# Performance work log

Hardware: AMD Instinct MI355X
Metric: run time of the kernel (lower is better)

Reference implementation:

```python
import jax, jax.numpy as jnp
import numpy as np

H = 8          # attention heads (all three convs)
N_NODES = 50000
N_EDGES = 800000
IN_DIM = 16
N_GRAPHS = 256


def _gat_layer(x, src, dst, W, a_src, a_dst, b, n_nodes):
    """PyG GATConv (concat=True, add_self_loops handled by caller via src/dst)."""
    f_out = a_src.shape[1]
    h = (x @ W).reshape(n_nodes, H, f_out)              # [N,H,F]
    al_s = jnp.einsum('nhf,hf->nh', h, a_src)           # [N,H]
    al_d = jnp.einsum('nhf,hf->nh', h, a_dst)           # [N,H]
    e = jax.nn.leaky_relu(al_s[src] + al_d[dst], 0.2)   # [E,H] per-edge logits
    # segment softmax over incoming edges of each destination node
    m = jax.ops.segment_max(e, dst, num_segments=n_nodes)
    m = jnp.where(jnp.isfinite(m), m, 0.0)
    p = jnp.exp(e - m[dst])
    s = jax.ops.segment_sum(p, dst, num_segments=n_nodes)
    alpha = p / (s[dst] + 1e-16)                        # [E,H]
    out = jax.ops.segment_sum(h[src] * alpha[:, :, None], dst, num_segments=n_nodes)
    return out.reshape(n_nodes, H * f_out) + b


def setup_inputs() -> dict:
    key = jax.random.key(0)
    ks = jax.random.split(key, 16)
    x = jax.random.normal(ks[0], (N_NODES, IN_DIM), dtype=jnp.float32)
    edge_index = jax.random.randint(ks[1], (2, N_EDGES), 0, N_NODES, dtype=jnp.int64)
    batch = jnp.sort(jax.random.randint(ks[2], (N_NODES,), 0, N_GRAPHS, dtype=jnp.int64))

    def glorot(k, shape):
        fan = shape[0] + shape[-1]
        return jax.random.normal(k, shape, dtype=jnp.float32) * np.sqrt(2.0 / fan)

    # conv1: 16 -> 8 heads x 8
    W1 = glorot(ks[3], (IN_DIM, H * 8))
    a_src1 = glorot(ks[4], (H, 8)); a_dst1 = glorot(ks[5], (H, 8))
    b1 = jnp.zeros((H * 8,), jnp.float32)
    # conv2: 64 -> 8 heads x 16
    W2 = glorot(ks[6], (64, H * 16))
    a_src2 = glorot(ks[7], (H, 16)); a_dst2 = glorot(ks[8], (H, 16))
    b2 = jnp.zeros((H * 16,), jnp.float32)
    # conv3: 128 -> 8 heads x 16
    W3 = glorot(ks[9], (128, H * 16))
    a_src3 = glorot(ks[10], (H, 16)); a_dst3 = glorot(ks[11], (H, 16))
    b3 = jnp.zeros((H * 16,), jnp.float32)

    fc1_w = glorot(ks[12], (128, 32)); fc1_b = jnp.zeros((32,), jnp.float32)
    fc2_w = glorot(ks[13], (32, 1));   fc2_b = jnp.zeros((1,), jnp.float32)

    return dict(x=x, edge_index=edge_index, batch=batch,
                W1=W1, a_src1=a_src1, a_dst1=a_dst1, b1=b1,
                W2=W2, a_src2=a_src2, a_dst2=a_dst2, b2=b2,
                W3=W3, a_src3=a_src3, a_dst3=a_dst3, b3=b3,
                fc1_w=fc1_w, fc1_b=fc1_b, fc2_w=fc2_w, fc2_b=fc2_b)


def reference(x, edge_index, batch,
              W1, a_src1, a_dst1, b1,
              W2, a_src2, a_dst2, b2,
              W3, a_src3, a_dst3, b3,
              fc1_w, fc1_b, fc2_w, fc2_b):
    n = x.shape[0]
    loops = jnp.arange(n, dtype=edge_index.dtype)        # GATConv add_self_loops=True
    src = jnp.concatenate([edge_index[0], loops])
    dst = jnp.concatenate([edge_index[1], loops])

    # eval mode: the F.dropout calls are no-ops
    h = jax.nn.elu(_gat_layer(x, src, dst, W1, a_src1, a_dst1, b1, n))
    h = jax.nn.elu(_gat_layer(h, src, dst, W2, a_src2, a_dst2, b2, n))
    h = jax.nn.elu(_gat_layer(h, src, dst, W3, a_src3, a_dst3, b3, n))

    # global_mean_pool over graph ids
    cnt = jax.ops.segment_sum(jnp.ones((n,), h.dtype), batch, num_segments=N_GRAPHS)
    pooled = jax.ops.segment_sum(h, batch, num_segments=N_GRAPHS) / jnp.maximum(cnt, 1.0)[:, None]

    out = jax.nn.relu(pooled @ fc1_w + fc1_b)
    return out @ fc2_w + fc2_b                            # [N_GRAPHS, 1]
```

## Files before the change

### kernel.cpp

```cpp
#include <hip/hip_runtime.h>
#include <hip/hip_bf16.h>
#include <cstdint>
#include <cstddef>

#define GAT_H 8
#define KBMAX 256
#define BCAP  6144
#define SB    8

typedef short bf16x8 __attribute__((ext_vector_type(8)));
typedef float f32x4  __attribute__((ext_vector_type(4)));

__device__ __forceinline__ unsigned bf16r(float x) {
    const unsigned u = __float_as_uint(x);
    return (u + 0x7fffu + ((u >> 16) & 1u)) >> 16;
}
#define B2F_LO(u) __uint_as_float((u) << 16)
#define B2F_HI(u) __uint_as_float((u) & 0xffff0000u)


__global__ __launch_bounds__(256) void bkt_scatter(const int* __restrict__ ei,
                                                   int* __restrict__ bwoff,
                                                   unsigned* __restrict__ staging,
                                                   float* __restrict__ Mh,
                                                   int nE, int nN, int kb) {
    __shared__ int cnt[KBMAX];
    __shared__ int gb[KBMAX];
    const int tid = threadIdx.x;
    if (blockIdx.x == 0 && tid < 3 * GAT_H) Mh[tid] = 0.f;
    cnt[tid] = 0;
    __syncthreads();
    const int base = blockIdx.x * 2048;
    const int ET = nE + nN;
    unsigned pk[8]; int bb[8], lr[8];
    #pragma unroll
    for (int k = 0; k < 8; ++k) {
        const int e = base + k * 256 + tid;
        bb[k] = -1;
        if (e < ET) {
            int src, dst;
            if (e < nE) { src = ei[e]; dst = ei[nE + e]; }
            else        { src = dst = e - nE; }
            pk[k] = ((unsigned)dst << 16) | (unsigned)src;
            bb[k] = dst >> 8;
            lr[k] = atomicAdd(&cnt[bb[k]], 1);
        }
    }
    __syncthreads();
    if (tid < kb)
        gb[tid] = cnt[tid] ? atomicAdd(&bwoff[tid], cnt[tid]) : 0;
    __syncthreads();
    #pragma unroll
    for (int k = 0; k < 8; ++k)
        if (bb[k] >= 0) {
            const int pos = gb[bb[k]] + lr[k];
            if (pos < BCAP)
                staging[(size_t)bb[k] * BCAP + pos] = pk[k];
        }
}

__global__ __launch_bounds__(1024) void bkt_build(const unsigned* __restrict__ staging,
                                                  const int* __restrict__ bwoff,
                                                  int* __restrict__ rowptr,
                                                  int* __restrict__ esrc, int N, int kb) {
    __shared__ int hist[256 * SB];
    __shared__ int run[256 * SB];
    __shared__ int sc[KBMAX];
    __shared__ int wt[4];
    __shared__ int wsum[16];
    __shared__ int outv[BCAP];
    const int b = blockIdx.x;
    const int tid = threadIdx.x;
    const int lane = tid & 63, wid = tid >> 6;

    if (tid < KBMAX) sc[tid] = (tid < kb) ? bwoff[tid] : 0;
    for (int i = tid; i < 256 * SB; i += 1024) { hist[i] = 0; run[i] = 0; }
    __syncthreads();

    if (tid < 256) {
        int incl = sc[tid];
        #pragma unroll
        for (int d = 1; d < 64; d <<= 1) {
            const int t2 = __shfl_up(incl, d, 64);
            if (lane >= d) incl += t2;
        }
        if (lane == 63) wt[wid] = incl;
        sc[tid] = incl;
    }
    __syncthreads();
    if (tid < 256) {
        int add = 0;
        #pragma unroll
        for (int w = 0; w < 4; ++w) if (w < wid) add += wt[w];
        sc[tid] += add;
    }
    __syncthreads();
    const int lo   = b ? sc[b - 1] : 0;
    const int cntb = sc[b] - lo;
    const int d0 = b << 8;
    const int nd = min(256, N - d0);
    const unsigned* stg = staging + (size_t)b * BCAP;
    const int lim = min(cntb, BCAP);

    for (int i = tid; i < lim; i += 1024) {
        const unsigned p = stg[i];
        const int dl = (int)(p >> 16) - d0;
        const int q  = (int)(p & 0xffffu) >> 13;
        atomicAdd(&hist[dl * SB + q], 1);
    }
    __syncthreads();

    const int b0 = hist[2 * tid], b1 = hist[2 * tid + 1];
    const int ps = b0 + b1;
    int incl = ps;
    #pragma unroll
    for (int d = 1; d < 64; d <<= 1) {
        const int t2 = __shfl_up(incl, d, 64);
        if (lane >= d) incl += t2;
    }
    if (lane == 63) wsum[wid] = incl;
    __syncthreads();
    if (tid == 0) {
        int runng = 0;
        #pragma unroll
        for (int w = 0; w < 16; ++w) { const int t2 = wsum[w]; wsum[w] = runng; runng += t2; }
    }
    __syncthreads();
    const int excl = wsum[wid] + incl - ps;
    hist[2 * tid]     = excl;
    hist[2 * tid + 1] = excl + b0;
    __syncthreads();

    if (tid < nd)
        rowptr[d0 + tid + 1] = lo + ((tid < 255) ? hist[(tid + 1) * SB] : cntb);
    if (b == 0 && tid == 0) rowptr[0] = 0;

    for (int i = tid; i < lim; i += 1024) {
        const unsigned p = stg[i];
        const int dl = (int)(p >> 16) - d0;
        const int q  = (int)(p & 0xffffu) >> 13;
        const int bin = dl * SB + q;
        const int pos = hist[bin] + atomicAdd(&run[bin], 1);
        if (pos < BCAP) outv[pos] = (int)(p & 0xffffu);
    }
    __syncthreads();
    for (int i = tid; i < lim; i += 1024) esrc[lo + i] = outv[i];
}


__global__ void wconv_kernel(const float* __restrict__ W, unsigned short* __restrict__ Wt, int D) {
    const int t = blockIdx.x * blockDim.x + threadIdx.x;
    if (t >= 128 * D) return;
    const int c = t / D, k = t % D;
    Wt[t] = (unsigned short)bf16r(W[(size_t)k * 128 + c]);
}


template<int D>
__global__ __launch_bounds__(256) void matmul_mfma(
        const unsigned short* __restrict__ X,
        const unsigned short* __restrict__ Wt,
        unsigned short* __restrict__ Hb,
        int N) {
    constexpr int DP = D + 8;
    __shared__ unsigned short xs[64 * DP];
    __shared__ unsigned short wsh[128 * DP];
    const int tid = threadIdx.x;
    const int n0 = blockIdx.x * 64;

    for (int t = tid; t < 64 * (D / 8); t += 256) {
        const int row = t / (D / 8), c8 = (t % (D / 8)) * 8;
        const int n = n0 + row;
        uint4 u = make_uint4(0u, 0u, 0u, 0u);
        if (n < N) u = *reinterpret_cast<const uint4*>(&X[(size_t)n * D + c8]);
        *reinterpret_cast<uint4*>(&xs[row * DP + c8]) = u;
    }
    for (int t = tid; t < 128 * (D / 8); t += 256) {
        const int row = t / (D / 8), c8 = (t % (D / 8)) * 8;
        *reinterpret_cast<uint4*>(&wsh[row * DP + c8]) =
            *reinterpret_cast<const uint4*>(&Wt[(size_t)row * D + c8]);
    }
    __syncthreads();

    const int w = tid >> 6, l = tid & 63;
    const int lr = l & 15, lk = l >> 4;
    f32x4 acc[8];
    #pragma unroll
    for (int j = 0; j < 8; ++j) acc[j] = (f32x4){0.f, 0.f, 0.f, 0.f};

    #pragma unroll
    for (int ks = 0; ks < D / 32; ++ks) {
        const int kb = ks * 32 + lk * 8;
        const bf16x8 a = *reinterpret_cast<const bf16x8*>(&xs[(16 * w + lr) * DP + kb]);
        #pragma unroll
        for (int nt = 0; nt < 8; ++nt) {
            const bf16x8 bfr = *reinterpret_cast<const bf16x8*>(&wsh[(16 * nt + lr) * DP + kb]);
            acc[nt] = __builtin_amdgcn_mfma_f32_16x16x32_bf16(a, bfr, acc[nt], 0, 0, 0);
        }
    }

    #pragma unroll
    for (int nt = 0; nt < 8; ++nt) {
        #pragma unroll
        for (int r = 0; r < 4; ++r) {
            const int n = n0 + 16 * w + lk * 4 + r;
            if (n < N)
                Hb[(size_t)n * 128 + 16 * nt + lr] = (unsigned short)bf16r(acc[nt][r]);
        }
    }
}


__global__ __launch_bounds__(256) void attnlogit_kernel(
        const unsigned short* __restrict__ Hb,
        const float* __restrict__ a_src, const float* __restrict__ a_dst,
        float* __restrict__ als, float* __restrict__ ald,
        float* __restrict__ Mh, int N) {
    __shared__ float sh[256];
    const int t = blockIdx.x * 256 + threadIdx.x;
    const int tid = threadIdx.x;
    float s1 = -1e30f;
    if (t < N * GAT_H) {
        const int h = t & 7;
        union { uint4 q[2]; unsigned w[8]; } v;
        const uint4* hp = reinterpret_cast<const uint4*>(Hb + (size_t)t * 16);
        v.q[0] = hp[0]; v.q[1] = hp[1];
        float a1 = 0.f, a2 = 0.f;
        #pragma unroll
        for (int j = 0; j < 8; ++j) {
            const float lo = B2F_LO(v.w[j]), hi2 = B2F_HI(v.w[j]);
            a1 += lo * a_src[h * 16 + 2 * j] + hi2 * a_src[h * 16 + 2 * j + 1];
            a2 += lo * a_dst[h * 16 + 2 * j] + hi2 * a_dst[h * 16 + 2 * j + 1];
        }
        als[t] = a1; ald[t] = a2;
        s1 = a1;
    }
    sh[tid] = s1;
    __syncthreads();
    #pragma unroll
    for (int off = 128; off >= 8; off >>= 1) {
        if (tid < off) sh[tid] = fmaxf(sh[tid], sh[tid + off]);
        __syncthreads();
    }
    if (tid < 8) {
        const float v2 = sh[tid];
        if (v2 > 0.f) atomicMax((int*)&Mh[tid], __float_as_int(v2));
    }
}


template<int D, int C, int KK, int F>
__global__ __launch_bounds__(256) void matmul_fused(
        const float* __restrict__ X, const float* __restrict__ W,
        const float* __restrict__ a_src, const float* __restrict__ a_dst,
        unsigned short* __restrict__ Hb,
        float* __restrict__ als, float* __restrict__ ald,
        float* __restrict__ Mh, int N) {
    constexpr int CG  = C / 8;
    constexpr int NGR = 256 / CG;
    constexpr int NPT = 64 / NGR;
    constexpr int XS  = KK + 4;
    __shared__ float xs[64][XS];
    __shared__ float wsh[KK][C];
    __shared__ int bmax[GAT_H];

    const int n0 = blockIdx.x * 64;
    const int tid = threadIdx.x;
    const int cg = tid % CG, ngr = tid / CG;
    const int c0 = cg * 8;
    if (tid < GAT_H) bmax[tid] = 0;

    float acc[NPT][8];
    #pragma unroll
    for (int i = 0; i < NPT; ++i)
        #pragma unroll
        for (int j = 0; j < 8; ++j) acc[i][j] = 0.f;

    for (int k0 = 0; k0 < D; k0 += KK) {
        for (int t = tid; t < 64 * (KK / 4); t += 256) {
            const int row = t / (KK / 4), c4 = (t % (KK / 4)) * 4;
            const int n = n0 + row;
            float4 v = make_float4(0.f, 0.f, 0.f, 0.f);
            if (n < N) v = *reinterpret_cast<const float4*>(&X[(size_t)n * D + k0 + c4]);
            *reinterpret_cast<float4*>(&xs[row][c4]) = v;
        }
        for (int t = tid; t < KK * (C / 4); t += 256) {
            const int row = t / (C / 4), c4 = (t % (C / 4)) * 4;
            *reinterpret_cast<float4*>(&wsh[row][c4]) =
                *reinterpret_cast<const float4*>(&W[(size_t)(k0 + row) * C + c4]);
        }
        __syncthreads();

        #pragma unroll
        for (int k4 = 0; k4 < KK; k4 += 4) {
            float4 xv[NPT];
            #pragma unroll
            for (int i = 0; i < NPT; ++i)
                xv[i] = *reinterpret_cast<const float4*>(&xs[ngr * NPT + i][k4]);
            #pragma unroll
            for (int kk = 0; kk < 4; ++kk) {
                const float4 w0 = *reinterpret_cast<const float4*>(&wsh[k4 + kk][c0]);
                const float4 w1 = *reinterpret_cast<const float4*>(&wsh[k4 + kk][c0 + 4]);
                #pragma unroll
                for (int i = 0; i < NPT; ++i) {
                    const float xk = (kk == 0) ? xv[i].x : (kk == 1) ? xv[i].y
                                   : (kk == 2) ? xv[i].z : xv[i].w;
                    acc[i][0] += xk * w0.x; acc[i][1] += xk * w0.y;
                    acc[i][2] += xk * w0.z; acc[i][3] += xk * w0.w;
                    acc[i][4] += xk * w1.x; acc[i][5] += xk * w1.y;
                    acc[i][6] += xk * w1.z; acc[i][7] += xk * w1.w;
                }
            }
        }
        __syncthreads();
    }

    const int h   = c0 / F;
    float asr[8], adr[8];
    #pragma unroll
    for (int q = 0; q < 8; ++q) {
        asr[q] = a_src[h * F + q];
        adr[q] = a_dst[h * F + q];
    }

    #pragma unroll
    for (int i = 0; i < NPT; ++i) {
        float s = 0.f, d2 = 0.f;
        #pragma unroll
        for (int q = 0; q < 8; ++q) { s += acc[i][q] * asr[q]; d2 += acc[i][q] * adr[q]; }
        const int n = n0 + ngr * NPT + i;
        if (n < N) {
            uint4 pk;
            pk.x = bf16r(acc[i][0]) | (bf16r(acc[i][1]) << 16);
            pk.y = bf16r(acc[i][2]) | (bf16r(acc[i][3]) << 16);
            pk.z = bf16r(acc[i][4]) | (bf16r(acc[i][5]) << 16);
            pk.w = bf16r(acc[i][6]) | (bf16r(acc[i][7]) << 16);
            *reinterpret_cast<uint4*>(&Hb[(size_t)n * C + c0]) = pk;
            als[(size_t)n * GAT_H + h] = s;
            ald[(size_t)n * GAT_H + h] = d2;
            if (s > 0.f) atomicMax(&bmax[h], __float_as_int(s));
        }
    }
    __syncthreads();
    if (tid < GAT_H) {
        const int v = bmax[tid];
        if (v > 0) atomicMax((int*)&Mh[tid], v);
    }
}


template<int F>
__global__ void gat_gather(const int* __restrict__ rowptr, const int* __restrict__ esrc,
                           const float* __restrict__ als, const float* __restrict__ ald,
                           const float* __restrict__ Mh,
                           const unsigned short* __restrict__ Hb, const float* __restrict__ b,
                           unsigned short* __restrict__ outb, int N) {
    const int t = blockIdx.x * blockDim.x + threadIdx.x;
    if (t >= N * GAT_H) return;
    const int dst = t >> 3, h = t & 7;
    const int beg = rowptr[dst], end = rowptr[dst + 1];
    const float adh = ald[t];
    float bnd = Mh[h] + adh;
    bnd = bnd > 0.f ? bnd : 0.2f * bnd;

    constexpr int NW = F / 2;
    float s = 0.f;
    float acc[F];
    #pragma unroll
    for (int j = 0; j < F; ++j) acc[j] = 0.f;

    int i = beg;
    for (; i + 1 < end; i += 2) {
        const int sa = esrc[i], sb = esrc[i + 1];
        const float ala = als[sa * GAT_H + h];
        const float alb = als[sb * GAT_H + h];
        union { uint4 q[NW / 4]; unsigned w[NW]; } va, vb;
        const uint4* ha  = reinterpret_cast<const uint4*>(Hb + ((size_t)sa * GAT_H + h) * F);
        const uint4* hb2 = reinterpret_cast<const uint4*>(Hb + ((size_t)sb * GAT_H + h) * F);
        #pragma unroll
        for (int j = 0; j < NW / 4; ++j) { va.q[j] = ha[j]; vb.q[j] = hb2[j]; }

        float xa = ala + adh; xa = xa > 0.f ? xa : 0.2f * xa;
        float xb = alb + adh; xb = xb > 0.f ? xb : 0.2f * xb;
        const float pa = __expf(xa - bnd);
        const float pb = __expf(xb - bnd);
        s += pa + pb;
        #pragma unroll
        for (int j = 0; j < NW; ++j) {
            acc[2 * j]     += pa * B2F_LO(va.w[j]) + pb * B2F_LO(vb.w[j]);
            acc[2 * j + 1] += pa * B2F_HI(va.w[j]) + pb * B2F_HI(vb.w[j]);
        }
    }
    if (i < end) {
        const int sa = esrc[i];
        const float ala = als[sa * GAT_H + h];
        union { uint4 q[NW / 4]; unsigned w[NW]; } va;
        const uint4* ha = reinterpret_cast<const uint4*>(Hb + ((size_t)sa * GAT_H + h) * F);
        #pragma unroll
        for (int j = 0; j < NW / 4; ++j) va.q[j] = ha[j];
        float xa = ala + adh; xa = xa > 0.f ? xa : 0.2f * xa;
        const float pa = __expf(xa - bnd);
        s += pa;
        #pragma unroll
        for (int j = 0; j < NW; ++j) {
            acc[2 * j]     += pa * B2F_LO(va.w[j]);
            acc[2 * j + 1] += pa * B2F_HI(va.w[j]);
        }
    }

    const float inv = 1.f / s;
    float val[F];
    #pragma unroll
    for (int j = 0; j < F; ++j) {
        const float v = acc[j] * inv + b[h * F + j];
        val[j] = v > 0.f ? v : expm1f(v);
    }
    #pragma unroll
    for (int j8 = 0; j8 < F / 8; ++j8) {
        uint4 pk;
        pk.x = bf16r(val[8 * j8 + 0]) | (bf16r(val[8 * j8 + 1]) << 16);
        pk.y = bf16r(val[8 * j8 + 2]) | (bf16r(val[8 * j8 + 3]) << 16);
        pk.z = bf16r(val[8 * j8 + 4]) | (bf16r(val[8 * j8 + 5]) << 16);
        pk.w = bf16r(val[8 * j8 + 6]) | (bf16r(val[8 * j8 + 7]) << 16);
        *reinterpret_cast<uint4*>(&outb[((size_t)dst * GAT_H + h) * F + 8 * j8]) = pk;
    }
}


__global__ __launch_bounds__(256) void pool_mlp_kernel(
        const unsigned short* __restrict__ Ab, const int* __restrict__ batch,
        const float* __restrict__ fc1w, const float* __restrict__ fc1b,
        const float* __restrict__ fc2w, const float* __restrict__ fc2b,
        float* __restrict__ out, int N) {
    const int g = blockIdx.x;
    int lo, hi;
    {
        int l = 0, h2 = N;
        while (l < h2) { const int mid = (l + h2) >> 1; if (batch[mid] < g) l = mid + 1; else h2 = mid; }
        lo = l;
        h2 = N;
        while (l < h2) { const int mid = (l + h2) >> 1; if (batch[mid] < g + 1) l = mid + 1; else h2 = mid; }
        hi = l;
    }
    __shared__ float part[16][128];
    __shared__ float pl[128];
    __shared__ float red2[32];
    const int tid = threadIdx.x;
    const int c8 = (tid & 15) * 8, r = tid >> 4;
    float a8[8];
    #pragma unroll
    for (int j = 0; j < 8; ++j) a8[j] = 0.f;
    for (int n = lo + r; n < hi; n += 16) {
        const uint4 u = *reinterpret_cast<const uint4*>(&Ab[(size_t)n * 128 + c8]);
        a8[0] += B2F_LO(u.x); a8[1] += B2F_HI(u.x);
        a8[2] += B2F_LO(u.y); a8[3] += B2F_HI(u.y);
        a8[4] += B2F_LO(u.z); a8[5] += B2F_HI(u.z);
        a8[6] += B2F_LO(u.w); a8[7] += B2F_HI(u.w);
    }
    #pragma unroll
    for (int j = 0; j < 8; ++j) part[r][c8 + j] = a8[j];
    __syncthreads();
    if (tid < 128) {
        float s = 0.f;
        #pragma unroll
        for (int rr = 0; rr < 16; ++rr) s += part[rr][tid];
        pl[tid] = s / fmaxf((float)(hi - lo), 1.f);
    }
    __syncthreads();
    if (tid < 32) {
        float a = fc1b[tid];
        for (int k = 0; k < 128; ++k) a += pl[k] * fc1w[k * 32 + tid];
        a = fmaxf(a, 0.f);
        red2[tid] = a * fc2w[tid];
    }
    __syncthreads();
    if (tid == 0) {
        float sum = fc2b[0];
        for (int k = 0; k < 32; ++k) sum += red2[k];
        out[g] = sum;
    }
}


extern "C" void kernel_launch(void* const* d_in, const int* in_sizes, int n_in,
                              void* d_out, int out_size, void* d_ws, size_t ws_size,
                              hipStream_t stream) {
    const float* x     = (const float*)d_in[0];
    const int*   ei    = (const int*)  d_in[1];
    const int*   batch = (const int*)  d_in[2];
    const float* W1 = (const float*)d_in[3],  *as1 = (const float*)d_in[4],
               *ad1 = (const float*)d_in[5],  *b1  = (const float*)d_in[6];
    const float* W2 = (const float*)d_in[7],  *as2 = (const float*)d_in[8],
               *ad2 = (const float*)d_in[9],  *b2  = (const float*)d_in[10];
    const float* W3 = (const float*)d_in[11], *as3 = (const float*)d_in[12],
               *ad3 = (const float*)d_in[13], *b3  = (const float*)d_in[14];
    const float* fc1w = (const float*)d_in[15], *fc1b = (const float*)d_in[16];
    const float* fc2w = (const float*)d_in[17], *fc2b = (const float*)d_in[18];

    const int N  = in_sizes[0] / 16;
    const int NE = in_sizes[1] / 2;
    const int NG = out_size;
    const int ET = NE + N;
    const int KB = (N + 255) >> 8;

    float* ws = (float*)d_ws;
    size_t off = 0;
    unsigned short* Ab = (unsigned short*)(ws + off); off += (size_t)N * 64;
    unsigned short* Hb = (unsigned short*)(ws + off); off += (size_t)N * 64;
    float* als  = ws + off; off += (size_t)N * GAT_H;
    float* ald  = ws + off; off += (size_t)N * GAT_H;
    float* Mh   = ws + off; off += 3 * GAT_H;
    int* rowptr = (int*)(ws + off); off += N + 1;
    int* esrc   = (int*)(ws + off); off += ET;
    unsigned* staging = (unsigned*)(ws + off); off += (size_t)KB * BCAP;
    int* bwoff  = (int*)(ws + off); off += KBMAX;
    unsigned short* Wt2 = (unsigned short*)(ws + off); off += 128 * 64 / 2;
    unsigned short* Wt3 = (unsigned short*)(ws + off); off += 128 * 128 / 2;

    hipMemsetAsync(bwoff, 0, KBMAX * sizeof(int), stream);
    bkt_scatter<<<(ET + 2047) / 2048, 256, 0, stream>>>(ei, bwoff, staging, Mh, NE, N, KB);
    bkt_build<<<KB, 1024, 0, stream>>>(staging, bwoff, rowptr, esrc, N, KB);
    wconv_kernel<<<(128 * 64 + 255) / 256, 256, 0, stream>>>(W2, Wt2, 64);
    wconv_kernel<<<(128 * 128 + 255) / 256, 256, 0, stream>>>(W3, Wt3, 128);

    const int NH = N * GAT_H;
    const int NHB = (NH + 255) / 256;
    const int NB = (N + 63) / 64;

    matmul_fused<16, 64, 16, 8><<<NB, 256, 0, stream>>>(x, W1, as1, ad1, Hb, als, ald, Mh, N);
    gat_gather<8><<<NHB, 256, 0, stream>>>(rowptr, esrc, als, ald, Mh, Hb, b1, Ab, N);

    matmul_mfma<64><<<NB, 256, 0, stream>>>(Ab, Wt2, Hb, N);
    attnlogit_kernel<<<NHB, 256, 0, stream>>>(Hb, as2, ad2, als, ald, Mh + GAT_H, N);
    gat_gather<16><<<NHB, 256, 0, stream>>>(rowptr, esrc, als, ald, Mh + GAT_H, Hb, b2, Ab, N);

    matmul_mfma<128><<<NB, 256, 0, stream>>>(Ab, Wt3, Hb, N);
    attnlogit_kernel<<<NHB, 256, 0, stream>>>(Hb, as3, ad3, als, ald, Mh + 2 * GAT_H, N);
    gat_gather<16><<<NHB, 256, 0, stream>>>(rowptr, esrc, als, ald, Mh + 2 * GAT_H, Hb, b3, Ab, N);

    pool_mlp_kernel<<<NG, 256, 0, stream>>>(Ab, batch, fc1w, fc1b, fc2w, fc2b,
                                            (float*)d_out, N);
}
```

Measured before the change: 233.1 us.

## Fuse attention-logit computation into MFMA matmul and coalesce H stores via LDS

Measured after the change: 218.5 us (median of 2 runs). 1.07x faster.

```diff
diff --git a/kernel.cpp b/kernel.cpp
--- a/kernel.cpp
+++ b/kernel.cpp
@@ -160,13 +160,19 @@
 __global__ __launch_bounds__(256) void matmul_mfma(
         const unsigned short* __restrict__ X,
         const unsigned short* __restrict__ Wt,
+        const float* __restrict__ a_src, const float* __restrict__ a_dst,
         unsigned short* __restrict__ Hb,
-        int N) {
+        float* __restrict__ als, float* __restrict__ ald,
+        float* __restrict__ Mh, int N) {
     constexpr int DP = D + 8;
+    constexpr int OP = 136;
+    static_assert(128 * DP >= 64 * OP, "wsh reuse too small");
     __shared__ unsigned short xs[64 * DP];
     __shared__ unsigned short wsh[128 * DP];
+    __shared__ int bmax[GAT_H];
     const int tid = threadIdx.x;
     const int n0 = blockIdx.x * 64;
+    if (tid < GAT_H) bmax[tid] = 0;
 
     for (int t = tid; t < 64 * (D / 8); t += 256) {
         const int row = t / (D / 8), c8 = (t % (D / 8)) * 8;
@@ -198,53 +204,56 @@
             acc[nt] = __builtin_amdgcn_mfma_f32_16x16x32_bf16(a, bfr, acc[nt], 0, 0, 0);
         }
     }
-
+    __syncthreads();
+
+    float asr[8], adr[8];
     #pragma unroll
     for (int nt = 0; nt < 8; ++nt) {
-        #pragma unroll
-        for (int r = 0; r < 4; ++r) {
-            const int n = n0 + 16 * w + lk * 4 + r;
-            if (n < N)
-                Hb[(size_t)n * 128 + 16 * nt + lr] = (unsigned short)bf16r(acc[nt][r]);
-        }
-    }
-}
-
-
-__global__ __launch_bounds__(256) void attnlogit_kernel(
-        const unsigned short* __restrict__ Hb,
-        const float* __restrict__ a_src, const float* __restrict__ a_dst,
-        float* __restrict__ als, float* __restrict__ ald,
-        float* __restrict__ Mh, int N) {
-    __shared__ float sh[256];
-    const int t = blockIdx.x * 256 + threadIdx.x;
-    const int tid = threadIdx.x;
-    float s1 = -1e30f;
-    if (t < N * GAT_H) {
-        const int h = t & 7;
-        union { uint4 q[2]; unsigned w[8]; } v;
-        const uint4* hp = reinterpret_cast<const uint4*>(Hb + (size_t)t * 16);
-        v.q[0] = hp[0]; v.q[1] = hp[1];
-        float a1 = 0.f, a2 = 0.f;
-        #pragma unroll
-        for (int j = 0; j < 8; ++j) {
-            const float lo = B2F_LO(v.w[j]), hi2 = B2F_HI(v.w[j]);
-            a1 += lo * a_src[h * 16 + 2 * j] + hi2 * a_src[h * 16 + 2 * j + 1];
-            a2 += lo * a_dst[h * 16 + 2 * j] + hi2 * a_dst[h * 16 + 2 * j + 1];
-        }
-        als[t] = a1; ald[t] = a2;
-        s1 = a1;
-    }
-    sh[tid] = s1;
-    __syncthreads();
-    #pragma unroll
-    for (int off = 128; off >= 8; off >>= 1) {
-        if (tid < off) sh[tid] = fmaxf(sh[tid], sh[tid + off]);
-        __syncthreads();
-    }
-    if (tid < 8) {
-        const float v2 = sh[tid];
-        if (v2 > 0.f) atomicMax((int*)&Mh[tid], __float_as_int(v2));
+        asr[nt] = a_src[nt * 16 + lr];
+        adr[nt] = a_dst[nt * 16 + lr];
+    }
+    float mys[4] = {0.f, 0.f, 0.f, 0.f}, myd[4] = {0.f, 0.f, 0.f, 0.f};
+    #pragma unroll
+    for (int r = 0; r < 4; ++r) {
+        #pragma unroll
+        for (int nt = 0; nt < 8; ++nt) {
+            float ps = acc[nt][r] * asr[nt];
+            float pd = acc[nt][r] * adr[nt];
+            #pragma unroll
+            for (int d = 1; d < 16; d <<= 1) {
+                ps += __shfl_xor(ps, d, 16);
+                pd += __shfl_xor(pd, d, 16);
+            }
+            if (lr == nt) { mys[r] = ps; myd[r] = pd; }
+        }
+    }
+    #pragma unroll
+    for (int r = 0; r < 4; ++r) {
+        const int n = n0 + 16 * w + lk * 4 + r;
+        if (lr < GAT_H && n < N) {
+            als[(size_t)n * GAT_H + lr] = mys[r];
+            ald[(size_t)n * GAT_H + lr] = myd[r];
+            if (mys[r] > 0.f) atomicMax(&bmax[lr], __float_as_int(mys[r]));
+        }
+    }
+
+    unsigned short* trp = wsh;
+    #pragma unroll
+    for (int nt = 0; nt < 8; ++nt)
+        #pragma unroll
+        for (int r = 0; r < 4; ++r)
+            trp[(16 * w + lk * 4 + r) * OP + 16 * nt + lr] = (unsigned short)bf16r(acc[nt][r]);
+    __syncthreads();
+    for (int t = tid; t < 64 * 16; t += 256) {
+        const int row = t >> 4, c8 = (t & 15) * 8;
+        const int n = n0 + row;
+        if (n < N)
+            *reinterpret_cast<uint4*>(&Hb[(size_t)n * 128 + c8]) =
+                *reinterpret_cast<const uint4*>(&trp[row * OP + c8]);
+    }
+    if (tid < GAT_H) {
+        const int v = bmax[tid];
+        if (v > 0) atomicMax((int*)&Mh[tid], v);
     }
 }
 
@@ -315,7 +324,7 @@
         __syncthreads();
     }
 
-    const int h   = c0 / F;
+    const int h = c0 / F;
     float asr[8], adr[8];
     #pragma unroll
     for (int q = 0; q < 8; ++q) {
@@ -530,12 +539,10 @@
     matmul_fused<16, 64, 16, 8><<<NB, 256, 0, stream>>>(x, W1, as1, ad1, Hb, als, ald, Mh, N);
     gat_gather<8><<<NHB, 256, 0, stream>>>(rowptr, esrc, als, ald, Mh, Hb, b1, Ab, N);
 
-    matmul_mfma<64><<<NB, 256, 0, stream>>>(Ab, Wt2, Hb, N);
-    attnlogit_kernel<<<NHB, 256, 0, stream>>>(Hb, as2, ad2, als, ald, Mh + GAT_H, N);
+    matmul_mfma<64><<<NB, 256, 0, stream>>>(Ab, Wt2, as2, ad2, Hb, als, ald, Mh + GAT_H, N);
     gat_gather<16><<<NHB, 256, 0, stream>>>(rowptr, esrc, als, ald, Mh + GAT_H, Hb, b2, Ab, N);
 
-    matmul_mfma<128><<<NB, 256, 0, stream>>>(Ab, Wt3, Hb, N);
-    attnlogit_kernel<<<NHB, 256, 0, stream>>>(Hb, as3, ad3, als, ald, Mh + 2 * GAT_H, N);
+    matmul_mfma<128><<<NB, 256, 0, stream>>>(Ab, Wt3, as3, ad3, Hb, als, ald, Mh + 2 * GAT_H, N);
     gat_gather<16><<<NHB, 256, 0, stream>>>(rowptr, esrc, als, ald, Mh + 2 * GAT_H, Hb, b3, Ab, N);
 
     pool_mlp_kernel<<<NG, 256, 0, stream>>>(Ab, batch, fc1w, fc1b, fc2w, fc2b,
```
